# Optimization experiments

Hardware: AMD Instinct MI355X
Metric: run time of the kernel (lower is better)

The kernel has to match this reference:

```python
import jax, jax.numpy as jnp
import numpy as np

TOP_K = 4

def setup_inputs() -> dict:
    key = jax.random.key(0)
    k1, k2, k3, k4 = jax.random.split(key, 4)
    B, S, D, E, H, O = 4, 2048, 1024, 8, 512, 1024
    x = jax.random.normal(k1, (B, S, D), dtype=jnp.float32)
    wg = jax.random.normal(k2, (E, D), dtype=jnp.float32) * 0.02
    w1 = jax.random.normal(k3, (E, H, D), dtype=jnp.float32) * 0.02
    w2 = jax.random.normal(k4, (E, O, H), dtype=jnp.float32) * 0.02
    return {"x": x, "wg": wg, "w1": w1, "w2": w2}

def reference(x, wg, w1, w2):
    # x: [B, S, D]; wg: [E, D]; w1: [E, H, D]; w2: [E, O, H]
    B, S, D = x.shape
    E = wg.shape[0]
    xt = x.reshape(B * S, D)                       # [N, D]
    logits = xt @ wg.T                              # [N, E] gate logits
    _, idx = jax.lax.top_k(logits, TOP_K)           # [N, k] selected experts
    N = xt.shape[0]
    # membership mask: 1.0 where expert e is among the token's top-k
    mask = jnp.zeros((N, E), dtype=x.dtype).at[jnp.arange(N)[:, None], idx].set(1.0)
    # dense per-expert FFN (relu MLP), then combine with unweighted sum over
    # the k selected experts (the original sums top-k outputs without gate weights)
    h = jax.nn.relu(jnp.einsum('nd,ehd->neh', xt, w1))   # [N, E, H]
    y = jnp.einsum('neh,eoh->neo', h, w2)                # [N, E, O]
    out = jnp.einsum('neo,ne->no', y, mask)              # [N, O]
    return out.reshape(B, S, -1)
```

## Files before the change

### kernel.cpp

```cpp
#include <hip/hip_runtime.h>

typedef float f32x4 __attribute__((ext_vector_type(4)));
typedef short bf16x8 __attribute__((ext_vector_type(8)));

#define NTOK 8192
#define DIM  1024
#define NE   8
#define NH   512
#define NO   1024

static __device__ __forceinline__ unsigned short f2bf(float f) {
  unsigned u = __float_as_uint(f);
  u += 0x7fffu + ((u >> 16) & 1u);
  return (unsigned short)(u >> 16);
}
static __device__ __forceinline__ unsigned pk2(float a, float b) {
  return (unsigned)f2bf(a) | ((unsigned)f2bf(b) << 16);
}

static __device__ __forceinline__ f32x4 mfma_bf16(bf16x8 a, bf16x8 b, f32x4 c) {
  return __builtin_amdgcn_mfma_f32_16x16x32_bf16(a, b, c, 0, 0, 0);
}

__global__ __launch_bounds__(256) void gate_kernel(
    const float* __restrict__ x, const float* __restrict__ wg,
    unsigned char* __restrict__ msk8, float* __restrict__ out)
{
  {
    size_t t = (size_t)blockIdx.x * 256 + threadIdx.x;
    float4* op = (float4*)(out + t * 16);
    float4 z4 = {0.f, 0.f, 0.f, 0.f};
    op[0] = z4; op[1] = z4; op[2] = z4; op[3] = z4;
  }
  const int lane = threadIdx.x & 63;
  const int wv = threadIdx.x >> 6;
  const int n = blockIdx.x * 4 + wv;
  const float* xr = x + (size_t)n * DIM;
  float4 v[4];
#pragma unroll
  for (int i = 0; i < 4; ++i) v[i] = *(const float4*)(xr + i * 256 + lane * 4);
  double logit[NE];
#pragma unroll
  for (int e = 0; e < NE; ++e) {
    const float* wr = wg + e * DIM;
    double s = 0.0;
#pragma unroll
    for (int i = 0; i < 4; ++i) {
      float4 g = *(const float4*)(wr + i * 256 + lane * 4);
      s += (double)v[i].x * g.x + (double)v[i].y * g.y +
           (double)v[i].z * g.z + (double)v[i].w * g.w;
    }
#pragma unroll
    for (int off = 32; off; off >>= 1) s += __shfl_down(s, off);
    logit[e] = s;
  }
  if (lane == 0) {
    unsigned sel = 0;
#pragma unroll
    for (int t = 0; t < 4; ++t) {
      int best = 0; double bv = -1.0e300;
#pragma unroll
      for (int e = 0; e < NE; ++e)
        if (!((sel >> e) & 1) && logit[e] > bv) { bv = logit[e]; best = e; }
      sel |= 1u << best;
    }
    msk8[n] = (unsigned char)sel;
  }
}

__global__ __launch_bounds__(256) void pack_w1_kernel(
    const float* __restrict__ w1, unsigned short* __restrict__ w1p)
{
  int t = blockIdx.x * 256 + threadIdx.x;
  int lane = t & 63, ks = (t >> 6) & 31, nt = (t >> 11) & 31, e = t >> 16;
  int r = nt * 16 + (lane & 15);
  int c = ks * 32 + (lane >> 4) * 8;
  const float* src = w1 + ((size_t)(e * 512 + r)) * 1024 + c;
  float4 f0 = *(const float4*)src;
  float4 f1 = *(const float4*)(src + 4);
  uint4 v;
  v.x = pk2(f0.x, f0.y); v.y = pk2(f0.z, f0.w);
  v.z = pk2(f1.x, f1.y); v.w = pk2(f1.z, f1.w);
  *(uint4*)(w1p + (size_t)t * 8) = v;
}

__global__ __launch_bounds__(256) void pack_w2_kernel(
    const float* __restrict__ w2, unsigned short* __restrict__ w2p)
{
  int t = blockIdx.x * 256 + threadIdx.x;
  int lane = t & 63, ks = (t >> 6) & 15, ot = (t >> 10) & 63, e = t >> 16;
  int o = ot * 16 + (lane & 15);
  int h = ks * 32 + (lane >> 4) * 8;
  const float* src = w2 + ((size_t)(e * 1024 + o)) * 512 + h;
  float4 f0 = *(const float4*)src;
  float4 f1 = *(const float4*)(src + 4);
  uint4 v;
  v.x = pk2(f0.x, f0.y); v.y = pk2(f0.z, f0.w);
  v.z = pk2(f1.x, f1.y); v.w = pk2(f1.z, f1.w);
  *(uint4*)(w2p + (size_t)t * 8) = v;
}

__global__ __launch_bounds__(1024, 4) void moe_ffn(
    const float* __restrict__ x, const unsigned short* __restrict__ w1p,
    const unsigned short* __restrict__ w2p, const unsigned char* __restrict__ msk8,
    float* __restrict__ out)
{
  __shared__ unsigned short xs[128 * 64 * 8];
  __shared__ unsigned short hs[32 * 64 * 8];

  const int tid = threadIdx.x;
  const int lane = tid & 63;
  const int wv = tid >> 6;
  const int row0 = (blockIdx.x >> 1) * 64;
  const int eq = blockIdx.x & 1;
  const int arow = lane & 15;
  const int kch = lane >> 4;

#pragma unroll
  for (int i = 0; i < 8; ++i) {
    int c = i * 1024 + tid;
    int r = c >> 7;
    int ch = c & 127;
    const float* src = x + (size_t)(row0 + r) * DIM + ch * 8;
    float4 f0 = *(const float4*)src;
    float4 f1 = *(const float4*)(src + 4);
    uint4 v;
    v.x = pk2(f0.x, f0.y); v.y = pk2(f0.z, f0.w);
    v.z = pk2(f1.x, f1.y); v.w = pk2(f1.z, f1.w);
    int f = (ch >> 2) * 4 + (r >> 4);
    int l = ((ch & 3) << 4) | (r & 15);
    *(uint4*)(xs + ((size_t)(f * 64 + l)) * 8) = v;
  }
  unsigned mb[4];
#pragma unroll
  for (int m = 0; m < 4; ++m)
    mb[m] = *(const unsigned*)(msk8 + row0 + m * 16 + kch * 4);
  __syncthreads();

  const unsigned short* xp = xs + lane * 8;
  const unsigned short* hp = hs + lane * 8;

  f32x4 oacc[4][4];
#pragma unroll
  for (int m = 0; m < 4; ++m)
#pragma unroll
    for (int n = 0; n < 4; ++n) oacc[m][n] = f32x4{0.f, 0.f, 0.f, 0.f};

#pragma unroll 1
  for (int el = 0; el < 4; ++el) {
    const int e = eq * 4 + el;

    f32x4 hacc0[4], hacc1[4];
#pragma unroll
    for (int m = 0; m < 4; ++m) {
      hacc0[m] = f32x4{0.f, 0.f, 0.f, 0.f};
      hacc1[m] = f32x4{0.f, 0.f, 0.f, 0.f};
    }
    const unsigned short* pb0 = w1p + ((size_t)(e * 32 + wv) * 32) * 512 + lane * 8;
    const unsigned short* pb1 = pb0 + (size_t)16 * 32 * 512;
#pragma unroll 4
    for (int ks = 0; ks < 32; ++ks) {
      bf16x8 b0 = *(const bf16x8*)(pb0 + ks * 512);
      bf16x8 b1 = *(const bf16x8*)(pb1 + ks * 512);
#pragma unroll
      for (int m = 0; m < 4; ++m) {
        bf16x8 a = *(const bf16x8*)(xp + (ks * 4 + m) * 512);
        hacc0[m] = mfma_bf16(a, b0, hacc0[m]);
        hacc1[m] = mfma_bf16(a, b1, hacc1[m]);
      }
    }

#pragma unroll
    for (int hh = 0; hh < 2; ++hh) {
      __syncthreads();

#pragma unroll
      for (int m = 0; m < 4; ++m)
#pragma unroll
        for (int j = 0; j < 4; ++j) {
          float hv = hh ? hacc1[m][j] : hacc0[m][j];
          float v = fmaxf(hv, 0.0f);
          v = ((mb[m] >> (j * 8 + e)) & 1u) ? v : 0.0f;
          int f = (wv >> 1) * 4 + m;
          int l2 = (((wv & 1) * 2 + (arow >> 3)) << 4) | (kch * 4 + j);
          hs[((size_t)(f * 64 + l2)) * 8 + (arow & 7)] = f2bf(v);
        }
      __syncthreads();

      const unsigned short* pc =
          w2p + ((size_t)((e * 64 + wv * 4) * 16 + hh * 8)) * 512 + lane * 8;
#pragma unroll 2
      for (int ks2 = 0; ks2 < 8; ++ks2) {
        bf16x8 a0 = *(const bf16x8*)(hp + (ks2 * 4 + 0) * 512);
        bf16x8 a1 = *(const bf16x8*)(hp + (ks2 * 4 + 1) * 512);
        bf16x8 a2 = *(const bf16x8*)(hp + (ks2 * 4 + 2) * 512);
        bf16x8 a3 = *(const bf16x8*)(hp + (ks2 * 4 + 3) * 512);
#pragma unroll
        for (int n = 0; n < 4; ++n) {
          bf16x8 b = *(const bf16x8*)(pc + (size_t)n * 8192 + ks2 * 512);
          oacc[0][n] = mfma_bf16(a0, b, oacc[0][n]);
          oacc[1][n] = mfma_bf16(a1, b, oacc[1][n]);
          oacc[2][n] = mfma_bf16(a2, b, oacc[2][n]);
          oacc[3][n] = mfma_bf16(a3, b, oacc[3][n]);
        }
      }
    }
  }

#pragma unroll
  for (int m = 0; m < 4; ++m)
#pragma unroll
    for (int n = 0; n < 4; ++n)
#pragma unroll
      for (int j = 0; j < 4; ++j) {
        int row = row0 + m * 16 + kch * 4 + j;
        int col = (wv * 4 + n) * 16 + arow;
        atomicAdd(&out[(size_t)row * NO + col], oacc[m][n][j]);
      }
}

extern "C" void kernel_launch(void* const* d_in, const int* in_sizes, int n_in,
                              void* d_out, int out_size, void* d_ws, size_t ws_size,
                              hipStream_t stream) {
  (void)in_sizes; (void)n_in; (void)out_size; (void)ws_size;
  const float* x  = (const float*)d_in[0];
  const float* wg = (const float*)d_in[1];
  const float* w1 = (const float*)d_in[2];
  const float* w2 = (const float*)d_in[3];
  float* out = (float*)d_out;
  char* ws = (char*)d_ws;
  unsigned short* w1p = (unsigned short*)ws;
  unsigned short* w2p = (unsigned short*)(ws + ((size_t)8 << 20));
  unsigned char* msk8 = (unsigned char*)(ws + ((size_t)16 << 20));

  gate_kernel<<<2048, 256, 0, stream>>>(x, wg, msk8, out);
  pack_w1_kernel<<<2048, 256, 0, stream>>>(w1, w1p);
  pack_w2_kernel<<<2048, 256, 0, stream>>>(w2, w2p);
  moe_ffn<<<256, 1024, 0, stream>>>(x, w1p, w2p, msk8, out);
}
```

Before: 219.4 us.

## Route tokens to per-expert lists and compute only selected experts

Adds a kernel that builds compacted per-expert token lists from the top-k mask. The FFN kernel then processes 64-token tiles of gathered tokens for one expert each and scatters results with atomics. This removes the dense evaluation of all eight experts per token, halving matrix work. In exchange it re-reads x per selected expert, adds a small serial list-building kernel, and doubles atomic traffic to the output.

Measured after the change: 241.8 us. 1.1x slower.

```diff
diff --git a/kernel.cpp b/kernel.cpp
--- a/kernel.cpp
+++ b/kernel.cpp
@@ -66,6 +66,46 @@
     }
     msk8[n] = (unsigned char)sel;
   }
+}
+
+__global__ __launch_bounds__(1024) void build_lists(
+    const unsigned char* __restrict__ msk8, int* __restrict__ lst,
+    int* __restrict__ cnt)
+{
+  __shared__ int wsum[16];
+  __shared__ int wpref[16];
+  __shared__ int base_s;
+  const int e = blockIdx.x;
+  const int tid = threadIdx.x;
+  const int lane = tid & 63, wv = tid >> 6;
+  if (tid == 0) base_s = 0;
+  __syncthreads();
+#pragma unroll 1
+  for (int c = 0; c < NTOK; c += 1024) {
+    int tok = c + tid;
+    int flag = (msk8[tok] >> e) & 1;
+    unsigned long long ball = __ballot(flag);
+    int lpref = __popcll(ball & ((1ull << lane) - 1ull));
+    int tot = __popcll(ball);
+    if (lane == 0) wsum[wv] = tot;
+    __syncthreads();
+    if (wv == 0 && lane < 16) {
+      int p = 0;
+      for (int k = 0; k < lane; ++k) p += wsum[k];
+      wpref[lane] = p;
+    }
+    __syncthreads();
+    int pos = base_s + wpref[wv] + lpref;
+    if (flag) lst[e * NTOK + pos] = tok;
+    __syncthreads();
+    if (tid == 0) {
+      int t = 0;
+      for (int k = 0; k < 16; ++k) t += wsum[k];
+      base_s += t;
+    }
+    __syncthreads();
+  }
+  if (tid == 0) cnt[e] = base_s;
 }
 
 __global__ __launch_bounds__(256) void pack_w1_kernel(
@@ -100,41 +140,47 @@
   *(uint4*)(w2p + (size_t)t * 8) = v;
 }
 
-__global__ __launch_bounds__(1024, 4) void moe_ffn(
+__global__ __launch_bounds__(1024, 4) void moe_expert(
     const float* __restrict__ x, const unsigned short* __restrict__ w1p,
-    const unsigned short* __restrict__ w2p, const unsigned char* __restrict__ msk8,
-    float* __restrict__ out)
+    const unsigned short* __restrict__ w2p, const int* __restrict__ lst,
+    const int* __restrict__ cnt, float* __restrict__ out)
 {
   __shared__ unsigned short xs[128 * 64 * 8];
   __shared__ unsigned short hs[32 * 64 * 8];
+
+  const int e = blockIdx.x & 7;
+  const int tile = blockIdx.x >> 3;
+  const int nct = cnt[e];
+  if (tile * 64 >= nct) return;
+  const int row0 = tile * 64;
 
   const int tid = threadIdx.x;
   const int lane = tid & 63;
   const int wv = tid >> 6;
-  const int row0 = (blockIdx.x >> 1) * 64;
-  const int eq = blockIdx.x & 1;
   const int arow = lane & 15;
   const int kch = lane >> 4;
+  const int* mylst = lst + e * NTOK;
 
 #pragma unroll
   for (int i = 0; i < 8; ++i) {
     int c = i * 1024 + tid;
     int r = c >> 7;
     int ch = c & 127;
-    const float* src = x + (size_t)(row0 + r) * DIM + ch * 8;
-    float4 f0 = *(const float4*)src;
-    float4 f1 = *(const float4*)(src + 4);
     uint4 v;
-    v.x = pk2(f0.x, f0.y); v.y = pk2(f0.z, f0.w);
-    v.z = pk2(f1.x, f1.y); v.w = pk2(f1.z, f1.w);
+    if (row0 + r < nct) {
+      int tok = mylst[row0 + r];
+      const float* src = x + (size_t)tok * DIM + ch * 8;
+      float4 f0 = *(const float4*)src;
+      float4 f1 = *(const float4*)(src + 4);
+      v.x = pk2(f0.x, f0.y); v.y = pk2(f0.z, f0.w);
+      v.z = pk2(f1.x, f1.y); v.w = pk2(f1.z, f1.w);
+    } else {
+      v = uint4{0u, 0u, 0u, 0u};
+    }
     int f = (ch >> 2) * 4 + (r >> 4);
     int l = ((ch & 3) << 4) | (r & 15);
     *(uint4*)(xs + ((size_t)(f * 64 + l)) * 8) = v;
   }
-  unsigned mb[4];
-#pragma unroll
-  for (int m = 0; m < 4; ++m)
-    mb[m] = *(const unsigned*)(msk8 + row0 + m * 16 + kch * 4);
   __syncthreads();
 
   const unsigned short* xp = xs + lane * 8;
@@ -146,16 +192,13 @@
 #pragma unroll
     for (int n = 0; n < 4; ++n) oacc[m][n] = f32x4{0.f, 0.f, 0.f, 0.f};
 
-#pragma unroll 1
-  for (int el = 0; el < 4; ++el) {
-    const int e = eq * 4 + el;
-
-    f32x4 hacc0[4], hacc1[4];
-#pragma unroll
-    for (int m = 0; m < 4; ++m) {
-      hacc0[m] = f32x4{0.f, 0.f, 0.f, 0.f};
-      hacc1[m] = f32x4{0.f, 0.f, 0.f, 0.f};
-    }
+  f32x4 hacc0[4], hacc1[4];
+#pragma unroll
+  for (int m = 0; m < 4; ++m) {
+    hacc0[m] = f32x4{0.f, 0.f, 0.f, 0.f};
+    hacc1[m] = f32x4{0.f, 0.f, 0.f, 0.f};
+  }
+  {
     const unsigned short* pb0 = w1p + ((size_t)(e * 32 + wv) * 32) * 512 + lane * 8;
     const unsigned short* pb1 = pb0 + (size_t)16 * 32 * 512;
 #pragma unroll 4
@@ -169,54 +212,57 @@
         hacc1[m] = mfma_bf16(a, b1, hacc1[m]);
       }
     }
-
-#pragma unroll
-    for (int hh = 0; hh < 2; ++hh) {
-      __syncthreads();
-
-#pragma unroll
-      for (int m = 0; m < 4; ++m)
-#pragma unroll
-        for (int j = 0; j < 4; ++j) {
-          float hv = hh ? hacc1[m][j] : hacc0[m][j];
-          float v = fmaxf(hv, 0.0f);
-          v = ((mb[m] >> (j * 8 + e)) & 1u) ? v : 0.0f;
-          int f = (wv >> 1) * 4 + m;
-          int l2 = (((wv & 1) * 2 + (arow >> 3)) << 4) | (kch * 4 + j);
-          hs[((size_t)(f * 64 + l2)) * 8 + (arow & 7)] = f2bf(v);
+  }
+
+#pragma unroll
+  for (int hh = 0; hh < 2; ++hh) {
+    __syncthreads();
+
+#pragma unroll
+    for (int m = 0; m < 4; ++m)
+#pragma unroll
+      for (int j = 0; j < 4; ++j) {
+        float hv = hh ? hacc1[m][j] : hacc0[m][j];
+        float v = fmaxf(hv, 0.0f);
+        int fr = (wv >> 1) * 4 + m;
+        int l2 = (((wv & 1) * 2 + (arow >> 3)) << 4) | (kch * 4 + j);
+        hs[((size_t)(fr * 64 + l2)) * 8 + (arow & 7)] = f2bf(v);
+      }
+    __syncthreads();
+
+    const unsigned short* pc =
+        w2p + ((size_t)((e * 64 + wv * 4) * 16 + hh * 8)) * 512 + lane * 8;
+#pragma unroll 2
+    for (int ks2 = 0; ks2 < 8; ++ks2) {
+      bf16x8 a0 = *(const bf16x8*)(hp + (ks2 * 4 + 0) * 512);
+      bf16x8 a1 = *(const bf16x8*)(hp + (ks2 * 4 + 1) * 512);
+      bf16x8 a2 = *(const bf16x8*)(hp + (ks2 * 4 + 2) * 512);
+      bf16x8 a3 = *(const bf16x8*)(hp + (ks2 * 4 + 3) * 512);
+#pragma unroll
+      for (int n = 0; n < 4; ++n) {
+        bf16x8 b = *(const bf16x8*)(pc + (size_t)n * 8192 + ks2 * 512);
+        oacc[0][n] = mfma_bf16(a0, b, oacc[0][n]);
+        oacc[1][n] = mfma_bf16(a1, b, oacc[1][n]);
+        oacc[2][n] = mfma_bf16(a2, b, oacc[2][n]);
+        oacc[3][n] = mfma_bf16(a3, b, oacc[3][n]);
+      }
+    }
+  }
+
+#pragma unroll
+  for (int m = 0; m < 4; ++m)
+#pragma unroll
+    for (int j = 0; j < 4; ++j) {
+      int g = row0 + m * 16 + kch * 4 + j;
+      if (g < nct) {
+        int tok = mylst[g];
+#pragma unroll
+        for (int n = 0; n < 4; ++n) {
+          int col = (wv * 4 + n) * 16 + arow;
+          atomicAdd(&out[(size_t)tok * NO + col], oacc[m][n][j]);
         }
-      __syncthreads();
-
-      const unsigned short* pc =
-          w2p + ((size_t)((e * 64 + wv * 4) * 16 + hh * 8)) * 512 + lane * 8;
-#pragma unroll 2
-      for (int ks2 = 0; ks2 < 8; ++ks2) {
-        bf16x8 a0 = *(const bf16x8*)(hp + (ks2 * 4 + 0) * 512);
-        bf16x8 a1 = *(const bf16x8*)(hp + (ks2 * 4 + 1) * 512);
-        bf16x8 a2 = *(const bf16x8*)(hp + (ks2 * 4 + 2) * 512);
-        bf16x8 a3 = *(const bf16x8*)(hp + (ks2 * 4 + 3) * 512);
-#pragma unroll
-        for (int n = 0; n < 4; ++n) {
-          bf16x8 b = *(const bf16x8*)(pc + (size_t)n * 8192 + ks2 * 512);
-          oacc[0][n] = mfma_bf16(a0, b, oacc[0][n]);
-          oacc[1][n] = mfma_bf16(a1, b, oacc[1][n]);
-          oacc[2][n] = mfma_bf16(a2, b, oacc[2][n]);
-          oacc[3][n] = mfma_bf16(a3, b, oacc[3][n]);
-        }
-      }
-    }
-  }
-
-#pragma unroll
-  for (int m = 0; m < 4; ++m)
-#pragma unroll
-    for (int n = 0; n < 4; ++n)
-#pragma unroll
-      for (int j = 0; j < 4; ++j) {
-        int row = row0 + m * 16 + kch * 4 + j;
-        int col = (wv * 4 + n) * 16 + arow;
-        atomicAdd(&out[(size_t)row * NO + col], oacc[m][n][j]);
-      }
+      }
+    }
 }
 
 extern "C" void kernel_launch(void* const* d_in, const int* in_sizes, int n_in,
@@ -232,9 +278,12 @@
   unsigned short* w1p = (unsigned short*)ws;
   unsigned short* w2p = (unsigned short*)(ws + ((size_t)8 << 20));
   unsigned char* msk8 = (unsigned char*)(ws + ((size_t)16 << 20));
+  int* lst = (int*)(ws + ((size_t)16 << 20) + 8192);
+  int* cnt = (int*)(ws + ((size_t)16 << 20) + 8192 + NE * NTOK * 4);
 
   gate_kernel<<<2048, 256, 0, stream>>>(x, wg, msk8, out);
+  build_lists<<<NE, 1024, 0, stream>>>(msk8, lst, cnt);
   pack_w1_kernel<<<2048, 256, 0, stream>>>(w1, w1p);
   pack_w2_kernel<<<2048, 256, 0, stream>>>(w2, w2p);
-  moe_ffn<<<256, 1024, 0, stream>>>(x, w1p, w2p, msk8, out);
-}
+  moe_expert<<<NE * 128, 1024, 0, stream>>>(x, w1p, w2p, lst, cnt, out);
+}
```
